# Performance work log

Measured on AMD Instinct MI355X. Metric: run time of the kernel, lower is better.

## Reference

```python
import jax, jax.numpy as jnp
import numpy as np


def _mlp(x, W1, b1, W2, b2):
    # x: (B, M, T); torch MLPLayer: transpose(1,2) -> Linear -> Linear -> LeakyReLU -> transpose back
    h = jnp.einsum('bmt,hm->bht', x, W1) + b1[None, :, None]   # (B, H, T)
    y = jnp.einsum('bht,oh->bot', h, W2) + b2[None, :, None]   # (B, M, T)
    return jax.nn.leaky_relu(y, negative_slope=0.01)


def _calc_attn(q, k, v):
    # q: (B, M, Tq), k: (B, M, Tk), v: (B, M, Tk)
    Tq = q.shape[-1]
    qk = jnp.einsum('bmq,bmk->bqk', q, k)                       # (B, Tq, Tk)
    eye = jnp.eye(Tq, dtype=qk.dtype)                           # broadcasts: (Tq,Tq) or (1,1)
    logits = jnp.exp(qk - qk * eye / jnp.sqrt(jnp.asarray(Tq, qk.dtype)))
    scores = jax.nn.softmax(logits, axis=-1)
    return jnp.einsum('bqk,bmk->bmq', scores, v)                # (B, M, Tq)


def setup_inputs() -> dict:
    key = jax.random.key(0)
    B, M, T, H = 16, 128, 2048, 512
    ks = jax.random.split(key, 14)
    s = 0.02
    inp = {
        'pattern': jax.random.normal(ks[0], (B, M, T), jnp.float32),
        'value': jax.random.normal(ks[1], (B, M, T), jnp.float32),
        'kernel_size': 33,
    }
    names = ['q', 'k', 'o']
    for i, n in enumerate(names):
        inp['W%s1' % n] = jax.random.normal(ks[2 + 4 * i], (H, M), jnp.float32) * s
        inp['b%s1' % n] = jax.random.normal(ks[3 + 4 * i], (H,), jnp.float32) * s
        inp['W%s2' % n] = jax.random.normal(ks[4 + 4 * i], (M, H), jnp.float32) * s
        inp['b%s2' % n] = jax.random.normal(ks[5 + 4 * i], (M,), jnp.float32) * s
    return inp


def reference(pattern, value, kernel_size, Wq1, bq1, Wq2, bq2, Wk1, bk1, Wk2, bk2, Wo1, bo1, Wo2, bo2):
    query = _mlp(pattern, Wq1, bq1, Wq2, bq2)
    key = _mlp(pattern, Wk1, bk1, Wk2, bk2)
    # full (internal) attention
    attn_in = _calc_attn(query, key, value)                     # (B, M, T)
    rep_in = _mlp(attn_in, Wo1, bo1, Wo2, bo2)
    # windowed (external) attention
    T = query.shape[-1]
    cu = (kernel_size - 1) // 2
    q_w = query[..., T - 1 - cu : T - cu]                       # (B, M, 1)
    k_w = key[..., kernel_size - cu - 1 : T - cu - 2]           # (B, M, T-k-1)
    v_w = value[..., kernel_size : T - 1]                       # (B, M, T-k-1)
    attn_ex = _calc_attn(q_w, k_w, v_w)                         # (B, M, 1)
    rep_ex = _mlp(attn_ex, Wo1, bo1, Wo2, bo2)
    return jnp.concatenate([rep_in, rep_ex], axis=-1)           # (B, M, T+1)
```

## Files before the change

### kernel.cpp

```cpp
#include <hip/hip_runtime.h>
#include <math.h>

#define B_    16
#define M_    128
#define T_    2048
#define H_    512
#define TOUT_ 2049

typedef unsigned short u16;
typedef unsigned int   u32;
typedef __bf16 bf16x8 __attribute__((ext_vector_type(8)));
typedef float  f32x16 __attribute__((ext_vector_type(16)));
typedef u32    u32x4  __attribute__((ext_vector_type(4)));
typedef u32    u32x2  __attribute__((ext_vector_type(2)));

#define A_OFF     0
#define C_OFF     49152
#define MEAN_OFF  49536
#define AQKBF_OFF 51584
#define AOBF_OFF  67968
#define QT_OFF    76160
#define KT_OFF    (76160 + 2097152)
#define VB_OFF    (76160 + 2 * 2097152)

static __device__ __forceinline__ u16 f2bf(float f) {
  u32 u = __float_as_uint(f);
  u = (u + 0x7FFFu + ((u >> 16) & 1u)) >> 16;
  return (u16)u;
}
static __device__ __forceinline__ u32 pk2(float lo, float hi) {
  return (u32)f2bf(lo) | ((u32)f2bf(hi) << 16);
}
static __device__ __forceinline__ bf16x8 ldfrag(const u16* p) {
  return __builtin_bit_cast(bf16x8, *(const u32x4*)p);
}

__global__ __launch_bounds__(128) void fuse_weights_all(
    const float* __restrict__ W1q, const float* __restrict__ b1q,
    const float* __restrict__ W2q, const float* __restrict__ b2q,
    const float* __restrict__ W1k, const float* __restrict__ b1k,
    const float* __restrict__ W2k, const float* __restrict__ b2k,
    const float* __restrict__ W1o, const float* __restrict__ b1o,
    const float* __restrict__ W2o, const float* __restrict__ b2o,
    float* __restrict__ A, float* __restrict__ c,
    u16* __restrict__ Aqk_bf, u16* __restrict__ Ao_bf) {
  __shared__ float w2row[H_];
  int which = blockIdx.x >> 7;
  int o = blockIdx.x & 127;
  const float* W1 = which == 0 ? W1q : which == 1 ? W1k : W1o;
  const float* b1 = which == 0 ? b1q : which == 1 ? b1k : b1o;
  const float* W2 = which == 0 ? W2q : which == 1 ? W2k : W2o;
  const float* b2 = which == 0 ? b2q : which == 1 ? b2k : b2o;
  int m = threadIdx.x;
  for (int h = m; h < H_; h += 128) w2row[h] = W2[o * H_ + h];
  __syncthreads();
  float acc = 0.f;
  for (int h = 0; h < H_; ++h) acc = fmaf(w2row[h], W1[h * M_ + m], acc);
  A[which * 16384 + o * M_ + m] = acc;
  u16 ab = f2bf(acc);
  if (which == 0)      Aqk_bf[o * 128 + m] = ab;
  else if (which == 1) Aqk_bf[(128 + o) * 128 + m] = ab;
  else                 Ao_bf[o * 128 + m] = ab;
  if (m == 0) {
    float cc = b2[o];
    for (int h = 0; h < H_; ++h) cc = fmaf(w2row[h], b1[h], cc);
    c[which * 128 + o] = cc;
  }
}

#define XSTR 136

__global__ __launch_bounds__(256) void prep_kernel(
    const float* __restrict__ pattern, const u16* __restrict__ Aqk_bf,
    const float* __restrict__ cqk, u16* __restrict__ qT, u16* __restrict__ kT,
    const float* __restrict__ value, u16* __restrict__ vb,
    float* __restrict__ meanv) {
  __shared__ alignas(16) u16 sxs[64 * XSTR];
  int bx = blockIdx.x;
  int tid = threadIdx.x;

  if (bx >= 512) {
    int bm = bx - 512;
    float* red = (float*)sxs;
    const float* row = value + (size_t)bm * T_;
    int i0 = tid * 8;
    float4 a = *(const float4*)(row + i0);
    float4 bq = *(const float4*)(row + i0 + 4);
    u32x4 o = {pk2(a.x, a.y), pk2(a.z, a.w), pk2(bq.x, bq.y), pk2(bq.z, bq.w)};
    *(u32x4*)&vb[(size_t)bm * T_ + i0] = o;
    float vals[8] = {a.x, a.y, a.z, a.w, bq.x, bq.y, bq.z, bq.w};
    float s = 0.f;
#pragma unroll
    for (int j = 0; j < 8; ++j) {
      int idx = i0 + j;
      if (idx >= 33 && idx < T_ - 1) s += vals[j];
    }
    red[tid] = s;
    __syncthreads();
    for (int st = 128; st > 0; st >>= 1) {
      if (tid < st) red[tid] += red[tid + st];
      __syncthreads();
    }
    if (tid == 0) meanv[bm] = red[0] * (1.f / 2014.f);
    return;
  }

  int b = bx >> 5;
  int t0 = (bx & 31) * 64;
  int lane = tid & 63;
  int wv = tid >> 6;
  int l31 = lane & 31;
  int lh8 = (lane >> 5) * 8;

  bf16x8 afr[2][8];
#pragma unroll
  for (int i = 0; i < 2; ++i) {
    const u16* ap = Aqk_bf + ((2 * wv + i) * 32 + l31) * 128 + lh8;
#pragma unroll
    for (int s = 0; s < 8; ++s) afr[i][s] = ldfrag(ap + 16 * s);
  }

  {
    int mp = tid & 63;
    int tc = tid >> 6;
    const float* r0 = pattern + ((size_t)(b * M_ + 2 * mp)) * T_ + t0 + tc * 16;
    const float* r1 = r0 + T_;
    u32* xw = (u32*)sxs;
#pragma unroll
    for (int j = 0; j < 4; ++j) {
      float4 a = *(const float4*)(r0 + 4 * j);
      float4 bb = *(const float4*)(r1 + 4 * j);
      int tt = tc * 16 + 4 * j;
      xw[(tt + 0) * 68 + mp] = pk2(a.x, bb.x);
      xw[(tt + 1) * 68 + mp] = pk2(a.y, bb.y);
      xw[(tt + 2) * 68 + mp] = pk2(a.z, bb.z);
      xw[(tt + 3) * 68 + mp] = pk2(a.w, bb.w);
    }
  }
  __syncthreads();

#pragma unroll
  for (int tt = 0; tt < 2; ++tt) {
    bf16x8 bfr[8];
    const u16* bp = &sxs[(tt * 32 + l31) * XSTR + lh8];
#pragma unroll
    for (int s = 0; s < 8; ++s) bfr[s] = ldfrag(bp + 16 * s);
#pragma unroll
    for (int i = 0; i < 2; ++i) {
      f32x16 acc;
#pragma unroll
      for (int r = 0; r < 16; ++r) acc[r] = 0.f;
#pragma unroll
      for (int s = 0; s < 8; ++s)
        acc = __builtin_amdgcn_mfma_f32_32x32x16_bf16(afr[i][s], bfr[s], acc, 0, 0, 0);
      int ot = 2 * wv + i;
      u16* dst = (ot < 4) ? qT : kT;
      int ob = (ot & 3) * 32;
      size_t trow = ((size_t)(b * T_ + t0 + tt * 32 + l31)) * 128;
#pragma unroll
      for (int g = 0; g < 4; ++g) {
        int o0 = 8 * g + 4 * (lane >> 5);
        float v0 = acc[4 * g + 0] + cqk[ot * 32 + o0 + 0];
        float v1 = acc[4 * g + 1] + cqk[ot * 32 + o0 + 1];
        float v2 = acc[4 * g + 2] + cqk[ot * 32 + o0 + 2];
        float v3 = acc[4 * g + 3] + cqk[ot * 32 + o0 + 3];
        v0 = v0 > 0.f ? v0 : 0.01f * v0;
        v1 = v1 > 0.f ? v1 : 0.01f * v1;
        v2 = v2 > 0.f ? v2 : 0.01f * v2;
        v3 = v3 > 0.f ? v3 : 0.01f * v3;
        u32x2 w = {pk2(v0, v1), pk2(v2, v3)};
        *(u32x2*)(dst + trow + ob + o0) = w;
      }
    }
  }
}

#define QSTR 136
#define VSTR 72

__global__ __launch_bounds__(256, 3) void attn_mfma_kernel(
    const u16* __restrict__ qT, const u16* __restrict__ kT,
    const u16* __restrict__ vB, const u16* __restrict__ Ao_bf,
    const float* __restrict__ co, const float* __restrict__ Aofp,
    const float* __restrict__ meanv, float* __restrict__ out) {
  __shared__ alignas(16) u16 smem[26624];
  u16* ks  = smem;
  u16* vs  = smem + 8704;
  u16* qsw = smem + 17920;

  int b = blockIdx.y;
  int q0 = blockIdx.x * 64;
  int tid = threadIdx.x;
  int lane = tid & 63;
  int wv = tid >> 6;
  int l31 = lane & 31;
  int lh8 = (lane >> 5) * 8;

  {
    const u16* gq = qT + (size_t)(b * T_ + q0) * 128;
#pragma unroll
    for (int it = 0; it < 4; ++it) {
      int r = it * 16 + (tid >> 4);
      int cm = (tid & 15) * 8;
      *(u32x4*)&qsw[r * QSTR + cm] = *(const u32x4*)&gq[r * 128 + cm];
    }
  }
  __syncthreads();

  int qw = (wv >> 1) * 32;
  int kw = (wv & 1) * 32;
  bf16x8 afrag[8];
  {
    const u16* qrow = &qsw[(qw + l31) * QSTR + lh8];
#pragma unroll
    for (int s = 0; s < 8; ++s) afrag[s] = ldfrag(qrow + s * 16);
  }

  int qt = wv & 1;
  int mb = (wv >> 1) * 2;

  f32x16 pacc[2];
  float dreg[16];
#pragma unroll
  for (int i = 0; i < 16; ++i) { pacc[0][i] = 0.f; pacc[1][i] = 0.f; dreg[i] = 0.f; }

  const u16* gkb = kT + (size_t)b * T_ * 128;
  const u16* gvb = vB + (size_t)b * M_ * T_;
  int kr = tid >> 4, kc = (tid & 15) * 8;
  int vr = tid >> 3, vc = (tid & 7) * 8;
  u32x4 kreg[4], vreg[4];
#pragma unroll
  for (int it = 0; it < 4; ++it) {
    kreg[it] = *(const u32x4*)&gkb[(size_t)(it * 16 + kr) * 128 + kc];
    vreg[it] = *(const u32x4*)&gvb[(size_t)(it * 32 + vr) * T_ + vc];
  }

  for (int kt = 0; kt < T_ / 64; ++kt) {
    int k0 = kt * 64;
    __syncthreads();
#pragma unroll
    for (int it = 0; it < 4; ++it) {
      *(u32x4*)&ks[(it * 16 + kr) * QSTR + kc] = kreg[it];
      *(u32x4*)&vs[(it * 32 + vr) * VSTR + vc] = vreg[it];
    }
    __syncthreads();

    {
      int kn = (kt < T_ / 64 - 1) ? k0 + 64 : k0;
#pragma unroll
      for (int it = 0; it < 4; ++it) {
        kreg[it] = *(const u32x4*)&gkb[(size_t)(kn + it * 16 + kr) * 128 + kc];
        vreg[it] = *(const u32x4*)&gvb[(size_t)(it * 32 + vr) * T_ + kn + vc];
      }
    }

    f32x16 sacc;
#pragma unroll
    for (int i = 0; i < 16; ++i) sacc[i] = 0.f;
    {
      const u16* krow = &ks[(kw + l31) * QSTR + lh8];
#pragma unroll
      for (int s = 0; s < 8; ++s) {
        bf16x8 bf = ldfrag(krow + s * 16);
        sacc = __builtin_amdgcn_mfma_f32_32x32x16_bf16(afrag[s], bf, sacc, 0, 0, 0);
      }
    }

    int kl = kw + l31;
    if (k0 == q0) {
#pragma unroll
      for (int r = 0; r < 16; ++r) {
        int qrow = qw + (r & 3) + 8 * (r >> 2) + 4 * (lane >> 5);
        if (qrow == kl) sacc[r] *= 0.97790291f;
      }
    }
#pragma unroll
    for (int r = 0; r < 16; ++r) {
      int qrow = qw + (r & 3) + 8 * (r >> 2) + 4 * (lane >> 5);
      float w = __expf(__expf(sacc[r]));
      u16 wb = f2bf(w);
      dreg[r] += __uint_as_float((u32)wb << 16);
      qsw[qrow * VSTR + kl] = wb;
    }
    __syncthreads();

#pragma unroll
    for (int s2 = 0; s2 < 4; ++s2) {
      bf16x8 wf = ldfrag(&qsw[(qt * 32 + l31) * VSTR + s2 * 16 + lh8]);
#pragma unroll
      for (int mi = 0; mi < 2; ++mi) {
        bf16x8 vf = ldfrag(&vs[((mb + mi) * 32 + l31) * VSTR + s2 * 16 + lh8]);
        pacc[mi] = __builtin_amdgcn_mfma_f32_32x32x16_bf16(vf, wf, pacc[mi], 0, 0, 0);
      }
    }
  }
  __syncthreads();

  float* dls = (float*)vs;
#pragma unroll
  for (int r = 0; r < 16; ++r) {
    float d = dreg[r];
    for (int off = 1; off < 32; off <<= 1) d += __shfl_xor(d, off, 64);
    dreg[r] = d;
  }
  if (l31 == 0) {
#pragma unroll
    for (int r = 0; r < 16; ++r) {
      int qrow = qw + (r & 3) + 8 * (r >> 2) + 4 * (lane >> 5);
      dls[(wv & 1) * 64 + qrow] = dreg[r];
    }
  }
  __syncthreads();

  {
    int qcol = qt * 32 + l31;
    float rden = 1.f / (dls[qcol] + dls[64 + qcol]);
#pragma unroll
    for (int mi = 0; mi < 2; ++mi) {
      int mbase = (mb + mi) * 32 + 4 * (lane >> 5);
#pragma unroll
      for (int g = 0; g < 4; ++g) {
        float v0 = pacc[mi][4 * g + 0] * rden;
        float v1 = pacc[mi][4 * g + 1] * rden;
        float v2 = pacc[mi][4 * g + 2] * rden;
        float v3 = pacc[mi][4 * g + 3] * rden;
        u32x2 w = {pk2(v0, v1), pk2(v2, v3)};
        *(u32x2*)&qsw[qcol * QSTR + mbase + 8 * g] = w;
      }
    }
  }
  __syncthreads();

  bf16x8 aofr[8];
  {
    const u16* ap = Ao_bf + (wv * 32 + l31) * 128 + lh8;
#pragma unroll
    for (int s = 0; s < 8; ++s) aofr[s] = ldfrag(ap + 16 * s);
  }
#pragma unroll
  for (int qt2 = 0; qt2 < 2; ++qt2) {
    bf16x8 pfr[8];
    const u16* pp = &qsw[(qt2 * 32 + l31) * QSTR + lh8];
#pragma unroll
    for (int s = 0; s < 8; ++s) pfr[s] = ldfrag(pp + 16 * s);
    f32x16 oacc;
#pragma unroll
    for (int r = 0; r < 16; ++r) oacc[r] = 0.f;
#pragma unroll
    for (int s = 0; s < 8; ++s)
      oacc = __builtin_amdgcn_mfma_f32_32x32x16_bf16(aofr[s], pfr[s], oacc, 0, 0, 0);
#pragma unroll
    for (int r = 0; r < 16; ++r) {
      int orow = wv * 32 + (r & 3) + 8 * (r >> 2) + 4 * (lane >> 5);
      float v = oacc[r] + co[orow];
      v = v > 0.f ? v : 0.01f * v;
      out[((size_t)(b * M_ + orow)) * TOUT_ + q0 + qt2 * 32 + l31] = v;
    }
  }

  if (q0 == 0 && tid < 128) {
    float acc = co[tid];
    const float* mv = meanv + b * 128;
    for (int m = 0; m < 128; ++m) acc = fmaf(Aofp[tid * 128 + m], mv[m], acc);
    acc = acc > 0.f ? acc : 0.01f * acc;
    out[((size_t)(b * M_ + tid)) * TOUT_ + 2048] = acc;
  }
}

extern "C" void kernel_launch(void* const* d_in, const int* in_sizes, int n_in,
                              void* d_out, int out_size, void* d_ws, size_t ws_size,
                              hipStream_t stream) {
  (void)in_sizes; (void)n_in; (void)out_size; (void)ws_size;
  const float* pattern = (const float*)d_in[0];
  const float* value   = (const float*)d_in[1];
  const float* Wq1 = (const float*)d_in[3];
  const float* bq1 = (const float*)d_in[4];
  const float* Wq2 = (const float*)d_in[5];
  const float* bq2 = (const float*)d_in[6];
  const float* Wk1 = (const float*)d_in[7];
  const float* bk1 = (const float*)d_in[8];
  const float* Wk2 = (const float*)d_in[9];
  const float* bk2 = (const float*)d_in[10];
  const float* Wo1 = (const float*)d_in[11];
  const float* bo1 = (const float*)d_in[12];
  const float* Wo2 = (const float*)d_in[13];
  const float* bo2 = (const float*)d_in[14];

  float* ws     = (float*)d_ws;
  float* A      = ws + A_OFF;
  float* c      = ws + C_OFF;
  float* meanv  = ws + MEAN_OFF;
  u16*   Aqk_bf = (u16*)(ws + AQKBF_OFF);
  u16*   Ao_bf  = (u16*)(ws + AOBF_OFF);
  u16*   qT     = (u16*)(ws + QT_OFF);
  u16*   kT     = (u16*)(ws + KT_OFF);
  u16*   vB     = (u16*)(ws + VB_OFF);
  float* out    = (float*)d_out;

  fuse_weights_all<<<384, 128, 0, stream>>>(
      Wq1, bq1, Wq2, bq2, Wk1, bk1, Wk2, bk2, Wo1, bo1, Wo2, bo2,
      A, c, Aqk_bf, Ao_bf);

  prep_kernel<<<512 + B_ * M_, 256, 0, stream>>>(
      pattern, Aqk_bf, c, qT, kT, value, vB, meanv);

  attn_mfma_kernel<<<dim3(T_ / 64, B_), 256, 0, stream>>>(
      qT, kT, vB, Ao_bf, c + 256, A + 32768, meanv, out);
}
```

Before: 202.7 us.

## Load K/V fragments directly from global into registers, restage prep transpose via LDS

The attention kernel drops LDS staging of K and V tiles. Each wave now loads its MFMA fragments straight from global memory into registers, with K prefetched one tile ahead, which removes one barrier per iteration and shrinks shared memory. Occupancy hint drops from 3 to 2 blocks per CU. The prep kernel now stages fp32 pattern tiles in LDS and writes q/k outputs through an LDS buffer so global stores are coalesced 16-byte rows, and the weight-fusion kernel parallelises the bias reduction and keeps only the fp32 output-MLP matrix.

Result: slower. 265.7 us (+31.1%).

```diff
diff --git a/kernel.cpp b/kernel.cpp
--- a/kernel.cpp
+++ b/kernel.cpp
@@ -15,13 +15,13 @@
 typedef u32    u32x2  __attribute__((ext_vector_type(2)));
 
 #define A_OFF     0
-#define C_OFF     49152
-#define MEAN_OFF  49536
-#define AQKBF_OFF 51584
-#define AOBF_OFF  67968
-#define QT_OFF    76160
-#define KT_OFF    (76160 + 2097152)
-#define VB_OFF    (76160 + 2 * 2097152)
+#define C_OFF     16384
+#define MEAN_OFF  16896
+#define AQKBF_OFF 19200
+#define AOBF_OFF  35584
+#define QT_OFF    43776
+#define KT_OFF    (43776 + 2097152)
+#define VB_OFF    (43776 + 2 * 2097152)
 
 static __device__ __forceinline__ u16 f2bf(float f) {
   u32 u = __float_as_uint(f);
@@ -55,33 +55,35 @@
   for (int h = m; h < H_; h += 128) w2row[h] = W2[o * H_ + h];
   __syncthreads();
   float acc = 0.f;
+#pragma unroll 8
   for (int h = 0; h < H_; ++h) acc = fmaf(w2row[h], W1[h * M_ + m], acc);
-  A[which * 16384 + o * M_ + m] = acc;
   u16 ab = f2bf(acc);
   if (which == 0)      Aqk_bf[o * 128 + m] = ab;
   else if (which == 1) Aqk_bf[(128 + o) * 128 + m] = ab;
-  else                 Ao_bf[o * 128 + m] = ab;
-  if (m == 0) {
-    float cc = b2[o];
-    for (int h = 0; h < H_; ++h) cc = fmaf(w2row[h], b1[h], cc);
-    c[which * 128 + o] = cc;
-  }
-}
-
-#define XSTR 136
+  else               { Ao_bf[o * 128 + m] = ab; A[o * M_ + m] = acc; }
+  if (m < 64) {
+    float cc = 0.f;
+    for (int h = m; h < H_; h += 64) cc = fmaf(w2row[h], b1[h], cc);
+#pragma unroll
+    for (int off = 32; off > 0; off >>= 1) cc += __shfl_down(cc, off, 64);
+    if (m == 0) c[which * 128 + o] = cc + b2[o];
+  }
+}
+
+#define XS 68
 
 __global__ __launch_bounds__(256) void prep_kernel(
     const float* __restrict__ pattern, const u16* __restrict__ Aqk_bf,
     const float* __restrict__ cqk, u16* __restrict__ qT, u16* __restrict__ kT,
     const float* __restrict__ value, u16* __restrict__ vb,
     float* __restrict__ meanv) {
-  __shared__ alignas(16) u16 sxs[64 * XSTR];
+  __shared__ alignas(16) float xsf[128 * XS];
   int bx = blockIdx.x;
   int tid = threadIdx.x;
 
   if (bx >= 512) {
     int bm = bx - 512;
-    float* red = (float*)sxs;
+    float* red = xsf;
     const float* row = value + (size_t)bm * T_;
     int i0 = tid * 8;
     float4 a = *(const float4*)(row + i0);
@@ -120,31 +122,37 @@
     for (int s = 0; s < 8; ++s) afr[i][s] = ldfrag(ap + 16 * s);
   }
 
-  {
-    int mp = tid & 63;
-    int tc = tid >> 6;
-    const float* r0 = pattern + ((size_t)(b * M_ + 2 * mp)) * T_ + t0 + tc * 16;
-    const float* r1 = r0 + T_;
-    u32* xw = (u32*)sxs;
-#pragma unroll
-    for (int j = 0; j < 4; ++j) {
-      float4 a = *(const float4*)(r0 + 4 * j);
-      float4 bb = *(const float4*)(r1 + 4 * j);
-      int tt = tc * 16 + 4 * j;
-      xw[(tt + 0) * 68 + mp] = pk2(a.x, bb.x);
-      xw[(tt + 1) * 68 + mp] = pk2(a.y, bb.y);
-      xw[(tt + 2) * 68 + mp] = pk2(a.z, bb.z);
-      xw[(tt + 3) * 68 + mp] = pk2(a.w, bb.w);
-    }
-  }
-  __syncthreads();
-
+#pragma unroll
+  for (int rep = 0; rep < 8; ++rep) {
+    int m = rep * 16 + (tid >> 4);
+    int tc = (tid & 15) * 4;
+    float4 v = *(const float4*)&pattern[(size_t)(b * M_ + m) * T_ + t0 + tc];
+    *(float4*)&xsf[m * XS + tc] = v;
+  }
+  __syncthreads();
+
+  bf16x8 bfr[2][8];
 #pragma unroll
   for (int tt = 0; tt < 2; ++tt) {
-    bf16x8 bfr[8];
-    const u16* bp = &sxs[(tt * 32 + l31) * XSTR + lh8];
-#pragma unroll
-    for (int s = 0; s < 8; ++s) bfr[s] = ldfrag(bp + 16 * s);
+#pragma unroll
+    for (int s = 0; s < 8; ++s) {
+      float v0 = xsf[(s * 16 + lh8 + 0) * XS + tt * 32 + l31];
+      float v1 = xsf[(s * 16 + lh8 + 1) * XS + tt * 32 + l31];
+      float v2 = xsf[(s * 16 + lh8 + 2) * XS + tt * 32 + l31];
+      float v3 = xsf[(s * 16 + lh8 + 3) * XS + tt * 32 + l31];
+      float v4 = xsf[(s * 16 + lh8 + 4) * XS + tt * 32 + l31];
+      float v5 = xsf[(s * 16 + lh8 + 5) * XS + tt * 32 + l31];
+      float v6 = xsf[(s * 16 + lh8 + 6) * XS + tt * 32 + l31];
+      float v7 = xsf[(s * 16 + lh8 + 7) * XS + tt * 32 + l31];
+      u32x4 p = {pk2(v0, v1), pk2(v2, v3), pk2(v4, v5), pk2(v6, v7)};
+      bfr[tt][s] = __builtin_bit_cast(bf16x8, p);
+    }
+  }
+  __syncthreads();
+
+  u16* obuf = (u16*)xsf;
+#pragma unroll
+  for (int tt = 0; tt < 2; ++tt) {
 #pragma unroll
     for (int i = 0; i < 2; ++i) {
       f32x16 acc;
@@ -152,41 +160,45 @@
       for (int r = 0; r < 16; ++r) acc[r] = 0.f;
 #pragma unroll
       for (int s = 0; s < 8; ++s)
-        acc = __builtin_amdgcn_mfma_f32_32x32x16_bf16(afr[i][s], bfr[s], acc, 0, 0, 0);
+        acc = __builtin_amdgcn_mfma_f32_32x32x16_bf16(afr[i][s], bfr[tt][s], acc, 0, 0, 0);
       int ot = 2 * wv + i;
-      u16* dst = (ot < 4) ? qT : kT;
-      int ob = (ot & 3) * 32;
-      size_t trow = ((size_t)(b * T_ + t0 + tt * 32 + l31)) * 128;
-#pragma unroll
-      for (int g = 0; g < 4; ++g) {
-        int o0 = 8 * g + 4 * (lane >> 5);
-        float v0 = acc[4 * g + 0] + cqk[ot * 32 + o0 + 0];
-        float v1 = acc[4 * g + 1] + cqk[ot * 32 + o0 + 1];
-        float v2 = acc[4 * g + 2] + cqk[ot * 32 + o0 + 2];
-        float v3 = acc[4 * g + 3] + cqk[ot * 32 + o0 + 3];
-        v0 = v0 > 0.f ? v0 : 0.01f * v0;
-        v1 = v1 > 0.f ? v1 : 0.01f * v1;
-        v2 = v2 > 0.f ? v2 : 0.01f * v2;
-        v3 = v3 > 0.f ? v3 : 0.01f * v3;
-        u32x2 w = {pk2(v0, v1), pk2(v2, v3)};
-        *(u32x2*)(dst + trow + ob + o0) = w;
+      int t = tt * 32 + l31;
+#pragma unroll
+      for (int r = 0; r < 16; ++r) {
+        int orow = (r & 3) + 8 * (r >> 2) + 4 * (lane >> 5);
+        float v = acc[r] + cqk[ot * 32 + orow];
+        v = v > 0.f ? v : 0.01f * v;
+        obuf[t * 258 + ot * 32 + orow] = f2bf(v);
       }
     }
+  }
+  __syncthreads();
+
+  const u32* ob32 = (const u32*)obuf;
+#pragma unroll
+  for (int g = 0; g < 8; ++g) {
+    int G = wv * 8 + g;
+    int mat = G >> 4;
+    int t = (G & 15) * 4 + (lane >> 4);
+    int og2 = lane & 15;
+    int wbase = t * 129 + mat * 64 + og2 * 4;
+    u32x4 vv = {ob32[wbase], ob32[wbase + 1], ob32[wbase + 2], ob32[wbase + 3]};
+    u32* dst = (u32*)((mat ? kT : qT) + ((size_t)(b * T_ + t0 + t)) * 128) + og2 * 4;
+    *(u32x4*)dst = vv;
   }
 }
 
 #define QSTR 136
 #define VSTR 72
 
-__global__ __launch_bounds__(256, 3) void attn_mfma_kernel(
+__global__ __launch_bounds__(256, 2) void attn_mfma_kernel(
     const u16* __restrict__ qT, const u16* __restrict__ kT,
     const u16* __restrict__ vB, const u16* __restrict__ Ao_bf,
     const float* __restrict__ co, const float* __restrict__ Aofp,
     const float* __restrict__ meanv, float* __restrict__ out) {
-  __shared__ alignas(16) u16 smem[26624];
-  u16* ks  = smem;
-  u16* vs  = smem + 8704;
-  u16* qsw = smem + 17920;
+  __shared__ alignas(16) u16 qsw[64 * QSTR];
+  __shared__ alignas(16) u16 wsm[64 * VSTR];
+  __shared__ float dls[128];
 
   int b = blockIdx.y;
   int q0 = blockIdx.x * 64;
@@ -219,51 +231,39 @@
   int qt = wv & 1;
   int mb = (wv >> 1) * 2;
 
+  const u16* kbase  = kT + ((size_t)(b * T_ + kw + l31)) * 128 + lh8;
+  const u16* vbase0 = vB + ((size_t)(b * M_ + mb * 32 + l31)) * T_ + lh8;
+  const u16* vbase1 = vB + ((size_t)(b * M_ + (mb + 1) * 32 + l31)) * T_ + lh8;
+
   f32x16 pacc[2];
   float dreg[16];
 #pragma unroll
   for (int i = 0; i < 16; ++i) { pacc[0][i] = 0.f; pacc[1][i] = 0.f; dreg[i] = 0.f; }
 
-  const u16* gkb = kT + (size_t)b * T_ * 128;
-  const u16* gvb = vB + (size_t)b * M_ * T_;
-  int kr = tid >> 4, kc = (tid & 15) * 8;
-  int vr = tid >> 3, vc = (tid & 7) * 8;
-  u32x4 kreg[4], vreg[4];
-#pragma unroll
-  for (int it = 0; it < 4; ++it) {
-    kreg[it] = *(const u32x4*)&gkb[(size_t)(it * 16 + kr) * 128 + kc];
-    vreg[it] = *(const u32x4*)&gvb[(size_t)(it * 32 + vr) * T_ + vc];
-  }
-
+  bf16x8 kf[8], vf[8];
+#pragma unroll
+  for (int s = 0; s < 8; ++s) kf[s] = ldfrag(kbase + s * 16);
+
+#pragma unroll 1
   for (int kt = 0; kt < T_ / 64; ++kt) {
     int k0 = kt * 64;
-    __syncthreads();
-#pragma unroll
-    for (int it = 0; it < 4; ++it) {
-      *(u32x4*)&ks[(it * 16 + kr) * QSTR + kc] = kreg[it];
-      *(u32x4*)&vs[(it * 32 + vr) * VSTR + vc] = vreg[it];
-    }
-    __syncthreads();
+#pragma unroll
+    for (int s2 = 0; s2 < 4; ++s2) {
+      vf[s2]     = ldfrag(vbase0 + k0 + s2 * 16);
+      vf[4 + s2] = ldfrag(vbase1 + k0 + s2 * 16);
+    }
+
+    f32x16 sacc;
+#pragma unroll
+    for (int i = 0; i < 16; ++i) sacc[i] = 0.f;
+#pragma unroll
+    for (int s = 0; s < 8; ++s)
+      sacc = __builtin_amdgcn_mfma_f32_32x32x16_bf16(afrag[s], kf[s], sacc, 0, 0, 0);
 
     {
-      int kn = (kt < T_ / 64 - 1) ? k0 + 64 : k0;
-#pragma unroll
-      for (int it = 0; it < 4; ++it) {
-        kreg[it] = *(const u32x4*)&gkb[(size_t)(kn + it * 16 + kr) * 128 + kc];
-        vreg[it] = *(const u32x4*)&gvb[(size_t)(it * 32 + vr) * T_ + kn + vc];
-      }
-    }
-
-    f32x16 sacc;
-#pragma unroll
-    for (int i = 0; i < 16; ++i) sacc[i] = 0.f;
-    {
-      const u16* krow = &ks[(kw + l31) * QSTR + lh8];
-#pragma unroll
-      for (int s = 0; s < 8; ++s) {
-        bf16x8 bf = ldfrag(krow + s * 16);
-        sacc = __builtin_amdgcn_mfma_f32_32x32x16_bf16(afrag[s], bf, sacc, 0, 0, 0);
-      }
+      size_t kn = (size_t)((kt < T_ / 64 - 1) ? k0 + 64 : k0) * 128;
+#pragma unroll
+      for (int s = 0; s < 8; ++s) kf[s] = ldfrag(kbase + kn + s * 16);
     }
 
     int kl = kw + l31;
@@ -280,23 +280,19 @@
       float w = __expf(__expf(sacc[r]));
       u16 wb = f2bf(w);
       dreg[r] += __uint_as_float((u32)wb << 16);
-      qsw[qrow * VSTR + kl] = wb;
+      wsm[qrow * VSTR + kl] = wb;
     }
     __syncthreads();
 
 #pragma unroll
     for (int s2 = 0; s2 < 4; ++s2) {
-      bf16x8 wf = ldfrag(&qsw[(qt * 32 + l31) * VSTR + s2 * 16 + lh8]);
-#pragma unroll
-      for (int mi = 0; mi < 2; ++mi) {
-        bf16x8 vf = ldfrag(&vs[((mb + mi) * 32 + l31) * VSTR + s2 * 16 + lh8]);
-        pacc[mi] = __builtin_amdgcn_mfma_f32_32x32x16_bf16(vf, wf, pacc[mi], 0, 0, 0);
-      }
-    }
-  }
-  __syncthreads();
-
-  float* dls = (float*)vs;
+      bf16x8 wf = ldfrag(&wsm[(qt * 32 + l31) * VSTR + s2 * 16 + lh8]);
+      pacc[0] = __builtin_amdgcn_mfma_f32_32x32x16_bf16(vf[s2],     wf, pacc[0], 0, 0, 0);
+      pacc[1] = __builtin_amdgcn_mfma_f32_32x32x16_bf16(vf[4 + s2], wf, pacc[1], 0, 0, 0);
+    }
+    __syncthreads();
+  }
+
 #pragma unroll
   for (int r = 0; r < 16; ++r) {
     float d = dreg[r];
@@ -405,5 +401,5 @@
       pattern, Aqk_bf, c, qT, kT, value, vB, meanv);
 
   attn_mfma_kernel<<<dim3(T_ / 64, B_), 256, 0, stream>>>(
-      qT, kT, vB, Ao_bf, c + 256, A + 32768, meanv, out);
-}
+      qT, kT, vB, Ao_bf, c + 256, A, meanv, out);
+}
```
